# Kernel optimization log

Hardware: AMD Instinct MI355X
Metric: run time of the kernel (lower is better)

## Reference

```python
import jax, jax.numpy as jnp
import numpy as np

DEGREE = 5
LN_EPS = 1e-5


def _xavier(key, shape):
    fan_in, fan_out = shape[-1] if len(shape) == 2 else shape[1] * shape[2], shape[0]
    limit = float(np.sqrt(6.0 / (fan_in + fan_out)))
    return jax.random.uniform(key, shape, jnp.float32, -limit, limit)


def setup_inputs() -> dict:
    key = jax.random.key(0)
    ks = jax.random.split(key, 6)
    B, D0, D1, D2 = 16384, 1024, 1024, 512
    return {
        "x": jax.random.normal(ks[0], (B, D0), jnp.float32),
        "coeff1": _xavier(ks[1], (D1, D0, DEGREE + 1)),
        "base_w1": _xavier(ks[2], (D1, D0)),
        "bias1": jnp.zeros((D1,), jnp.float32),
        "ln_gamma": jnp.ones((D1,), jnp.float32),
        "ln_beta": jnp.zeros((D1,), jnp.float32),
        "coeff2": _xavier(ks[3], (D2, D1, DEGREE + 1)),
        "base_w2": _xavier(ks[4], (D2, D1)),
        "bias2": jnp.zeros((D2,), jnp.float32),
    }


def _cheb_layer(x, coeff, base_w, bias):
    # x: [B, I]; coeff: [O, I, D+1]; base_w: [O, I]; bias: [O]
    xn = jnp.tanh(x)
    polys = [jnp.ones_like(xn), xn]
    for _ in range(2, DEGREE + 1):
        polys.append(2.0 * xn * polys[-1] - polys[-2])
    cheb = jnp.stack(polys, axis=-1)  # [B, I, D+1]
    y = jnp.einsum("bid,oid->bo", cheb, coeff)
    y = y + x @ base_w.T + bias
    return y


def _layernorm(h, gamma, beta):
    mu = jnp.mean(h, axis=-1, keepdims=True)
    var = jnp.mean(jnp.square(h - mu), axis=-1, keepdims=True)
    return (h - mu) * jax.lax.rsqrt(var + LN_EPS) * gamma + beta


def reference(x, coeff1, base_w1, bias1, ln_gamma, ln_beta, coeff2, base_w2, bias2):
    x = jnp.tanh(x)  # input_normalization='tanh'
    h = _cheb_layer(x, coeff1, base_w1, bias1)
    h = _layernorm(h, ln_gamma, ln_beta)
    h = h * jax.nn.sigmoid(h)  # SiLU
    out = _cheb_layer(h, coeff2, base_w2, bias2)
    return out
```

## Files before the change

kernel.cpp:

```cpp
#include <hip/hip_runtime.h>


typedef __bf16 bf16x8 __attribute__((ext_vector_type(8)));
typedef float f32x4 __attribute__((ext_vector_type(4)));
typedef unsigned short u16x8 __attribute__((ext_vector_type(8)));

__device__ __forceinline__ unsigned short f2bf(float f) {
    unsigned int u = __float_as_uint(f);
    unsigned int r = (u + 0x7FFFu + ((u >> 16) & 1u)) >> 16;
    return (unsigned short)r;
}
__device__ __forceinline__ float bf2f(unsigned short b) {
    return __uint_as_float(((unsigned int)b) << 16);
}

__device__ __forceinline__ float fast_tanh(float x) {
    float a = fminf(fmaxf(x, -15.f), 15.f);
    float e = __expf(2.f * a);
    return 1.f - 2.f * __builtin_amdgcn_rcpf(e + 1.f);
}
__device__ __forceinline__ float fast_silu(float y) {
    float a = fminf(fmaxf(y, -30.f), 30.f);
    return y * __builtin_amdgcn_rcpf(1.f + __expf(-a));
}

__device__ __forceinline__ void cheb_pack(float s, unsigned short* o6) {
    float u  = fast_tanh(s);
    float T1 = u;
    float T2 = 2.f * u * u - 1.f;
    float T3 = 2.f * u * T2 - T1;
    float T4 = 2.f * u * T3 - T2;
    float T5 = 2.f * u * T4 - T3;
    o6[0] = f2bf(T1); o6[1] = f2bf(T2); o6[2] = f2bf(T3);
    o6[3] = f2bf(T4); o6[4] = f2bf(T5); o6[5] = f2bf(s);
}

__device__ __forceinline__ void load_lds16(const void* g, void* l) {
    __builtin_amdgcn_global_load_lds(
        (const __attribute__((address_space(1))) void*)g,
        (__attribute__((address_space(3))) void*)l, 16, 0, 0);
}

__global__ __launch_bounds__(256) void prep_w_kernel(
    const float* __restrict__ coeff, const float* __restrict__ base_w,
    unsigned short* __restrict__ W, int OI)
{
    int idx = blockIdx.x * 256 + threadIdx.x;
    if (idx >= OI) return;
    const float* c = coeff + (size_t)idx * 6;
    unsigned short w0 = f2bf(c[1]), w1 = f2bf(c[2]), w2 = f2bf(c[3]),
                   w3 = f2bf(c[4]), w4 = f2bf(c[5]), w5 = f2bf(base_w[idx]);
    unsigned int* d = (unsigned int*)(W + (size_t)idx * 6);
    d[0] = w0 | ((unsigned int)w1 << 16);
    d[1] = w2 | ((unsigned int)w3 << 16);
    d[2] = w4 | ((unsigned int)w5 << 16);
}

__global__ __launch_bounds__(256) void prep_bias_kernel(
    const float* __restrict__ coeff, const float* __restrict__ bias,
    float* __restrict__ bp, int I)
{
    int o = blockIdx.x, tid = threadIdx.x;
    float s = 0.f;
    for (int i = tid; i < I; i += 256) s += coeff[((size_t)o * I + i) * 6];
    #pragma unroll
    for (int off = 32; off > 0; off >>= 1) s += __shfl_down(s, off);
    __shared__ float red[4];
    int lane = tid & 63, wv = tid >> 6;
    if (lane == 0) red[wv] = s;
    __syncthreads();
    if (tid == 0) bp[o] = bias[o] + red[0] + red[1] + red[2] + red[3];
}

__global__ __launch_bounds__(256) void expand1_kernel(
    const float* __restrict__ x, unsigned short* __restrict__ Xa)
{
    int b = blockIdx.x, tid = threadIdx.x;
    f32x4 xv = *(const f32x4*)(x + (size_t)b * 1024 + tid * 4);
    alignas(16) unsigned short ov[24];
    #pragma unroll
    for (int e = 0; e < 4; e++) cheb_pack(fast_tanh(xv[e]), ov + e * 6);
    u16x8* dst = (u16x8*)(Xa + (size_t)b * 6144 + tid * 24);
    const u16x8* src = (const u16x8*)ov;
    dst[0] = src[0]; dst[1] = src[1]; dst[2] = src[2];
}

__global__ __launch_bounds__(256) void ln_silu_expand_kernel(
    const unsigned short* __restrict__ H, const float* __restrict__ gamma,
    const float* __restrict__ beta, unsigned short* __restrict__ Xa)
{
    int b = blockIdx.x, tid = threadIdx.x;
    ushort4 hb = *(const ushort4*)(H + (size_t)b * 1024 + tid * 4);
    float hv[4] = { bf2f(hb.x), bf2f(hb.y), bf2f(hb.z), bf2f(hb.w) };
    float s1 = hv[0] + hv[1] + hv[2] + hv[3];
    float s2 = hv[0]*hv[0] + hv[1]*hv[1] + hv[2]*hv[2] + hv[3]*hv[3];
    #pragma unroll
    for (int off = 32; off > 0; off >>= 1) {
        s1 += __shfl_down(s1, off);
        s2 += __shfl_down(s2, off);
    }
    __shared__ float red[8];
    __shared__ float stats[2];
    int lane = tid & 63, wv = tid >> 6;
    if (lane == 0) { red[wv] = s1; red[4 + wv] = s2; }
    __syncthreads();
    if (tid == 0) {
        float t1 = red[0] + red[1] + red[2] + red[3];
        float t2 = red[4] + red[5] + red[6] + red[7];
        float mu = t1 * (1.f / 1024.f);
        float var = t2 * (1.f / 1024.f) - mu * mu;
        stats[0] = mu;
        stats[1] = rsqrtf(var + 1e-5f);
    }
    __syncthreads();
    float mu = stats[0], rs = stats[1];
    f32x4 g  = *(const f32x4*)(gamma + tid * 4);
    f32x4 bt = *(const f32x4*)(beta  + tid * 4);
    alignas(16) unsigned short ov[24];
    #pragma unroll
    for (int e = 0; e < 4; e++) {
        float y = (hv[e] - mu) * rs * g[e] + bt[e];
        cheb_pack(fast_silu(y), ov + e * 6);
    }
    u16x8* dst = (u16x8*)(Xa + (size_t)b * 6144 + tid * 24);
    const u16x8* src = (const u16x8*)ov;
    dst[0] = src[0]; dst[1] = src[1]; dst[2] = src[2];
}

#define FENCE() asm volatile("" ::: "memory")

#define PH_MID() do { \
    FENCE(); __builtin_amdgcn_s_barrier(); \
    asm volatile("s_waitcnt lgkmcnt(0)" ::: "memory"); \
    __builtin_amdgcn_sched_barrier(0); \
    __builtin_amdgcn_s_setprio(1); } while (0)

#define PH_END() do { \
    __builtin_amdgcn_s_setprio(0); \
    FENCE(); __builtin_amdgcn_s_barrier(); FENCE(); } while (0)

#define VM_STEADY() do { \
    if constexpr (BN == 256) asm volatile("s_waitcnt vmcnt(8)" ::: "memory"); \
    else                     asm volatile("s_waitcnt vmcnt(6)" ::: "memory"); } while (0)
#define VM_DRAIN() asm volatile("s_waitcnt vmcnt(0)" ::: "memory")

#define RD_A(DST0, DST1, BASE, MH) do { \
    _Pragma("unroll") \
    for (int mf = 0; mf < 4; ++mf) { \
        const unsigned short* p_ = (BASE) + ((MH) * 64 + mf * 16) * 64; \
        DST0[mf] = *(const bf16x8*)(p_ + c0); \
        DST1[mf] = *(const bf16x8*)(p_ + c1); \
    } } while (0)

#define RD_B(DST, BASE, CSEL) do { \
    _Pragma("unroll") \
    for (int nf = 0; nf < FN; ++nf) \
        DST[nf] = *(const bf16x8*)((BASE) + (nf * 16) * 64 + (CSEL)); \
    } while (0)

#define QUAD(MH, AV, BV) do { \
    _Pragma("unroll") \
    for (int mf = 0; mf < 4; ++mf) \
        _Pragma("unroll") \
        for (int nf = 0; nf < FN; ++nf) \
            acc[MH][mf][nf] = __builtin_amdgcn_mfma_f32_16x16x32_bf16( \
                AV[mf], BV[nf], acc[MH][mf][nf], 0, 0, 0); \
    } while (0)

template<int BN, bool OUT_BF16>
__global__ __launch_bounds__(512, 2) void gemm8_kernel(
    const unsigned short* __restrict__ A,
    const unsigned short* __restrict__ Wt,
    const float* __restrict__ bias,
    void* __restrict__ Cout,
    int N, int K, int NMT)
{
    constexpr int FN   = BN / 64;
    constexpr int BUPW = BN / 64;

    __shared__ __align__(16) unsigned short As[2 * 256 * 64];
    __shared__ __align__(16) unsigned short Bs[2 * BN * 64];

    const int tid  = threadIdx.x;
    const int lane = tid & 63;
    const int wave = tid >> 6;
    const int wm   = wave >> 2;
    const int wn   = wave & 3;

    int wg = blockIdx.x;
    {
        const int nwg = gridDim.x;
        if ((nwg & 7) == 0) {
            const int cpx = nwg >> 3;
            wg = (wg & 7) * cpx + (wg >> 3);
        }
    }
    const int mt = wg % NMT;
    const int nt = wg / NMT;
    const size_t m0 = (size_t)mt * 256;
    const size_t n0 = (size_t)nt * BN;

    const int srow   = lane >> 3;
    const int schunk = (lane & 7) ^ (srow & 7);
    const unsigned short* Ag = A  + (m0 + srow) * (size_t)K + schunk * 8;
    const unsigned short* Bg = Wt + (n0 + srow) * (size_t)K + schunk * 8;

    const int fr  = lane & 15;
    const int cg  = lane >> 4;
    const int fr7 = fr & 7;
    const int c0  = ((cg    ) ^ fr7) << 3;
    const int c1  = ((cg + 4) ^ fr7) << 3;

    const int NT = K >> 6;

    const unsigned short* A0f = As + fr * 64 + (wm * 128) * 64;
    const unsigned short* A1f = A0f + 256 * 64;
    const unsigned short* B0f = Bs + fr * 64 + (wn * (BN / 4)) * 64;
    const unsigned short* B1f = B0f + BN * 64;

    auto stageA = [&](int kt, int bsel) {
        const unsigned short* g = Ag + kt * 64;
        unsigned short* l = As + bsel * (256 * 64);
        #pragma unroll
        for (int j = 0; j < 4; ++j) {
            const int u = wave * 4 + j;
            load_lds16(g + (size_t)(u * 8) * K, l + u * 512);
        }
    };
    auto stageB = [&](int kt, int bsel) {
        const unsigned short* g = Bg + kt * 64;
        unsigned short* l = Bs + bsel * (BN * 64);
        #pragma unroll
        for (int j = 0; j < BUPW; ++j) {
            const int u = wave * BUPW + j;
            load_lds16(g + (size_t)(u * 8) * K, l + u * 512);
        }
    };

    f32x4 acc[2][4][FN];
    #pragma unroll
    for (int mh = 0; mh < 2; ++mh)
        #pragma unroll
        for (int mf = 0; mf < 4; ++mf)
            #pragma unroll
            for (int nf = 0; nf < FN; ++nf)
                acc[mh][mf][nf] = f32x4{0.f, 0.f, 0.f, 0.f};

    stageB(0, 0); stageA(0, 0);
    stageB(1, 1); stageA(1, 1);
    VM_STEADY();
    FENCE(); __builtin_amdgcn_s_barrier(); FENCE();

    for (int kt = 0; kt < NT; kt += 2) {
        const bool st = (kt + 4) <= NT;
        bf16x8 a0[4], a1[4], b0[FN], b1[FN];

        RD_A(a0, a1, A0f, 0);
        RD_B(b0, B0f, c0);
        PH_MID(); QUAD(0, a0, b0); PH_END();

        RD_B(b1, B0f, c1);
        PH_MID(); QUAD(0, a1, b1); PH_END();

        RD_A(a0, a1, A0f, 1);
        if (st) stageB(kt + 2, 0);
        PH_MID(); QUAD(1, a0, b0); PH_END();

        if (st) { stageA(kt + 2, 0); VM_STEADY(); }
        else    { VM_DRAIN(); }
        PH_MID(); QUAD(1, a1, b1); PH_END();

        RD_A(a0, a1, A1f, 0);
        RD_B(b0, B1f, c0);
        PH_MID(); QUAD(0, a0, b0); PH_END();

        RD_B(b1, B1f, c1);
        PH_MID(); QUAD(0, a1, b1); PH_END();

        RD_A(a0, a1, A1f, 1);
        if (st) stageB(kt + 3, 1);
        PH_MID(); QUAD(1, a0, b0); PH_END();

        if (st) { stageA(kt + 3, 1); VM_STEADY(); }
        else    { VM_DRAIN(); }
        PH_MID(); QUAD(1, a1, b1); PH_END();
    }

    const size_t rbase0 = m0 + wm * 128 + ((lane >> 4) << 2);
    const int cb = lane & 15;
    int colg[FN]; float bv[FN];
    #pragma unroll
    for (int nf = 0; nf < FN; ++nf) {
        colg[nf] = (int)n0 + wn * (BN / 4) + nf * 16 + cb;
        bv[nf] = bias[colg[nf]];
    }
    #pragma unroll
    for (int mh = 0; mh < 2; ++mh)
        #pragma unroll
        for (int mf = 0; mf < 4; ++mf) {
            const size_t rg0 = rbase0 + mh * 64 + mf * 16;
            #pragma unroll
            for (int r = 0; r < 4; ++r) {
                const size_t rowoff = (rg0 + r) * (size_t)N;
                #pragma unroll
                for (int nf = 0; nf < FN; ++nf) {
                    const float v = acc[mh][mf][nf][r] + bv[nf];
                    if constexpr (OUT_BF16)
                        ((unsigned short*)Cout)[rowoff + colg[nf]] = f2bf(v);
                    else
                        ((float*)Cout)[rowoff + colg[nf]] = v;
                }
            }
        }
}

extern "C" void kernel_launch(void* const* d_in, const int* in_sizes, int n_in,
                              void* d_out, int out_size, void* d_ws, size_t ws_size,
                              hipStream_t stream)
{
    const float* x       = (const float*)d_in[0];
    const float* coeff1  = (const float*)d_in[1];
    const float* base_w1 = (const float*)d_in[2];
    const float* bias1   = (const float*)d_in[3];
    const float* gamma   = (const float*)d_in[4];
    const float* beta    = (const float*)d_in[5];
    const float* coeff2  = (const float*)d_in[6];
    const float* base_w2 = (const float*)d_in[7];
    const float* bias2   = (const float*)d_in[8];
    float* out = (float*)d_out;

    const int B = 16384, D0 = 1024, D1 = 1024, D2 = 512;
    const int K1 = D0 * 6, K2 = D1 * 6;

    char* base = (char*)d_ws;
    size_t off = 0;
    unsigned short* W1 = (unsigned short*)(base + off); off += (size_t)D1 * K1 * 2;
    unsigned short* W2 = (unsigned short*)(base + off); off += (size_t)D2 * K2 * 2;
    float* b1p = (float*)(base + off); off += (size_t)D1 * 4;
    float* b2p = (float*)(base + off); off += (size_t)D2 * 4;
    off = (off + 255) & ~(size_t)255;

    size_t per_row = (size_t)K1 * 2 + (size_t)D1 * 2;
    long long avail = (long long)ws_size - (long long)off;
    long long mcl = avail > 0 ? avail / (long long)per_row : 0;
    int Mc = (int)((mcl / 256) * 256);
    if (Mc < 256) Mc = 256;
    if (Mc > B) Mc = B;

    unsigned short* Xa = (unsigned short*)(base + off);
    unsigned short* h = (unsigned short*)(base + off + (size_t)Mc * K1 * 2);

    prep_w_kernel<<<(D1 * D0 + 255) / 256, 256, 0, stream>>>(coeff1, base_w1, W1, D1 * D0);
    prep_w_kernel<<<(D2 * D1 + 255) / 256, 256, 0, stream>>>(coeff2, base_w2, W2, D2 * D1);
    prep_bias_kernel<<<D1, 256, 0, stream>>>(coeff1, bias1, b1p, D0);
    prep_bias_kernel<<<D2, 256, 0, stream>>>(coeff2, bias2, b2p, D1);

    for (int m0 = 0; m0 < B; m0 += Mc) {
        int rows = (B - m0 < Mc) ? (B - m0) : Mc;
        int nmt = rows / 256;
        expand1_kernel<<<rows, 256, 0, stream>>>(x + (size_t)m0 * D0, Xa);
        gemm8_kernel<256, true><<<nmt * (D1 / 256), 512, 0, stream>>>(
            Xa, W1, b1p, h, D1, K1, nmt);
        ln_silu_expand_kernel<<<rows, 256, 0, stream>>>(h, gamma, beta, Xa);
        gemm8_kernel<128, false><<<nmt * (D2 / 128), 512, 0, stream>>>(
            Xa, W2, b2p, out + (size_t)m0 * D2, D2, K2, nmt);
    }
}
```

Measured before the change: 678.8 us.

## Replace 8-phase GEMM schedule with simpler BK=32 double-buffered pipeline

Swaps the GEMM mainloop's 8-phase ping-pong schedule (BK=64, barriers and setprio around each MFMA quad) for a simpler loop with BK=32 tiles, two LDS buffers and register double-buffering of fragments. Each iteration waits for all outstanding loads, prefetches the next tile into registers and issues async global->LDS loads for a tile two steps ahead. The LDS layout and swizzle change to 32-wide rows. This halves the LDS footprint and cuts barrier overhead, but it issues full vmcnt(0) waits every step and exposes less latency per barrier.

```diff
diff --git a/kernel.cpp b/kernel.cpp
--- a/kernel.cpp
+++ b/kernel.cpp
@@ -127,59 +127,24 @@
     dst[0] = src[0]; dst[1] = src[1]; dst[2] = src[2];
 }
 
-#define FENCE() asm volatile("" ::: "memory")
-
-#define PH_MID() do { \
-    FENCE(); __builtin_amdgcn_s_barrier(); \
-    asm volatile("s_waitcnt lgkmcnt(0)" ::: "memory"); \
-    __builtin_amdgcn_sched_barrier(0); \
-    __builtin_amdgcn_s_setprio(1); } while (0)
-
-#define PH_END() do { \
-    __builtin_amdgcn_s_setprio(0); \
-    FENCE(); __builtin_amdgcn_s_barrier(); FENCE(); } while (0)
-
-#define VM_STEADY() do { \
-    if constexpr (BN == 256) asm volatile("s_waitcnt vmcnt(8)" ::: "memory"); \
-    else                     asm volatile("s_waitcnt vmcnt(6)" ::: "memory"); } while (0)
-#define VM_DRAIN() asm volatile("s_waitcnt vmcnt(0)" ::: "memory")
-
-#define RD_A(DST0, DST1, BASE, MH) do { \
-    _Pragma("unroll") \
-    for (int mf = 0; mf < 4; ++mf) { \
-        const unsigned short* p_ = (BASE) + ((MH) * 64 + mf * 16) * 64; \
-        DST0[mf] = *(const bf16x8*)(p_ + c0); \
-        DST1[mf] = *(const bf16x8*)(p_ + c1); \
-    } } while (0)
-
-#define RD_B(DST, BASE, CSEL) do { \
-    _Pragma("unroll") \
-    for (int nf = 0; nf < FN; ++nf) \
-        DST[nf] = *(const bf16x8*)((BASE) + (nf * 16) * 64 + (CSEL)); \
-    } while (0)
-
-#define QUAD(MH, AV, BV) do { \
-    _Pragma("unroll") \
-    for (int mf = 0; mf < 4; ++mf) \
-        _Pragma("unroll") \
-        for (int nf = 0; nf < FN; ++nf) \
-            acc[MH][mf][nf] = __builtin_amdgcn_mfma_f32_16x16x32_bf16( \
-                AV[mf], BV[nf], acc[MH][mf][nf], 0, 0, 0); \
-    } while (0)
+
+#define WAITTOP() do { \
+    asm volatile("s_waitcnt vmcnt(0) lgkmcnt(0)" ::: "memory"); \
+    __builtin_amdgcn_s_barrier(); } while (0)
 
 template<int BN, bool OUT_BF16>
-__global__ __launch_bounds__(512, 2) void gemm8_kernel(
+__global__ __launch_bounds__(512, 2) void gemm3_kernel(
     const unsigned short* __restrict__ A,
     const unsigned short* __restrict__ Wt,
     const float* __restrict__ bias,
     void* __restrict__ Cout,
     int N, int K, int NMT)
 {
-    constexpr int FN   = BN / 64;
-    constexpr int BUPW = BN / 64;
-
-    __shared__ __align__(16) unsigned short As[2 * 256 * 64];
-    __shared__ __align__(16) unsigned short Bs[2 * BN * 64];
+    constexpr int FN  = BN / 64;
+    constexpr int ASZ = 256 * 32;
+    constexpr int BSZ = BN * 32;
+    __shared__ __align__(16) unsigned short As[2 * ASZ];
+    __shared__ __align__(16) unsigned short Bs[2 * BSZ];
 
     const int tid  = threadIdx.x;
     const int lane = tid & 63;
@@ -190,52 +155,32 @@
     int wg = blockIdx.x;
     {
         const int nwg = gridDim.x;
-        if ((nwg & 7) == 0) {
-            const int cpx = nwg >> 3;
-            wg = (wg & 7) * cpx + (wg >> 3);
-        }
+        if ((nwg & 7) == 0) { const int cpx = nwg >> 3; wg = (wg & 7) * cpx + (wg >> 3); }
     }
     const int mt = wg % NMT;
     const int nt = wg / NMT;
     const size_t m0 = (size_t)mt * 256;
     const size_t n0 = (size_t)nt * BN;
 
-    const int srow   = lane >> 3;
-    const int schunk = (lane & 7) ^ (srow & 7);
-    const unsigned short* Ag = A  + (m0 + srow) * (size_t)K + schunk * 8;
-    const unsigned short* Bg = Wt + (n0 + srow) * (size_t)K + schunk * 8;
-
-    const int fr  = lane & 15;
-    const int cg  = lane >> 4;
-    const int fr7 = fr & 7;
-    const int c0  = ((cg    ) ^ fr7) << 3;
-    const int c1  = ((cg + 4) ^ fr7) << 3;
-
-    const int NT = K >> 6;
-
-    const unsigned short* A0f = As + fr * 64 + (wm * 128) * 64;
-    const unsigned short* A1f = A0f + 256 * 64;
-    const unsigned short* B0f = Bs + fr * 64 + (wn * (BN / 4)) * 64;
-    const unsigned short* B1f = B0f + BN * 64;
-
-    auto stageA = [&](int kt, int bsel) {
-        const unsigned short* g = Ag + kt * 64;
-        unsigned short* l = As + bsel * (256 * 64);
-        #pragma unroll
-        for (int j = 0; j < 4; ++j) {
-            const int u = wave * 4 + j;
-            load_lds16(g + (size_t)(u * 8) * K, l + u * 512);
-        }
-    };
-    auto stageB = [&](int kt, int bsel) {
-        const unsigned short* g = Bg + kt * 64;
-        unsigned short* l = Bs + bsel * (BN * 64);
-        #pragma unroll
-        for (int j = 0; j < BUPW; ++j) {
-            const int u = wave * BUPW + j;
-            load_lds16(g + (size_t)(u * 8) * K, l + u * 512);
-        }
-    };
+    const int cs   = (((lane & 3) ^ ((lane >> 3) & 3)) << 3);
+    const int srow = lane >> 2;
+    const unsigned short* AgJ0 = A + (m0 + (size_t)((wave * 2 + 0) * 16 + srow)) * K + cs;
+    const unsigned short* AgJ1 = A + (m0 + (size_t)((wave * 2 + 1) * 16 + srow)) * K + cs;
+    const unsigned short* BgJ0 = Wt + (n0 + (size_t)((wave * (BN / 128) + 0) * 16 + srow)) * K + cs;
+    const unsigned short* BgJ1 = (BN == 256)
+        ? Wt + (n0 + (size_t)((wave * 2 + 1) * 16 + srow)) * K + cs : BgJ0;
+    unsigned short* AD0 = As + (wave * 2 + 0) * 512 + lane * 8;
+    unsigned short* AD1 = As + (wave * 2 + 1) * 512 + lane * 8;
+    unsigned short* BD0 = Bs + (wave * (BN / 128) + 0) * 512 + lane * 8;
+    unsigned short* BD1 = Bs + (wave * 2 + 1) * 512 + lane * 8;
+
+    const int fr = lane & 15;
+    const int cg = lane >> 4;
+    const int ck = ((cg ^ ((fr >> 1) & 3)) << 3);
+    const unsigned short* PA = As + (wm * 128 + fr) * 32 + ck;
+    const unsigned short* PB = Bs + (wn * (BN / 4) + fr) * 32 + ck;
+
+    const int NT = K >> 5;
 
     f32x4 acc[2][4][FN];
     #pragma unroll
@@ -246,45 +191,64 @@
             for (int nf = 0; nf < FN; ++nf)
                 acc[mh][mf][nf] = f32x4{0.f, 0.f, 0.f, 0.f};
 
-    stageB(0, 0); stageA(0, 0);
-    stageB(1, 1); stageA(1, 1);
-    VM_STEADY();
-    FENCE(); __builtin_amdgcn_s_barrier(); FENCE();
-
-    for (int kt = 0; kt < NT; kt += 2) {
-        const bool st = (kt + 4) <= NT;
-        bf16x8 a0[4], a1[4], b0[FN], b1[FN];
-
-        RD_A(a0, a1, A0f, 0);
-        RD_B(b0, B0f, c0);
-        PH_MID(); QUAD(0, a0, b0); PH_END();
-
-        RD_B(b1, B0f, c1);
-        PH_MID(); QUAD(0, a1, b1); PH_END();
-
-        RD_A(a0, a1, A0f, 1);
-        if (st) stageB(kt + 2, 0);
-        PH_MID(); QUAD(1, a0, b0); PH_END();
-
-        if (st) { stageA(kt + 2, 0); VM_STEADY(); }
-        else    { VM_DRAIN(); }
-        PH_MID(); QUAD(1, a1, b1); PH_END();
-
-        RD_A(a0, a1, A1f, 0);
-        RD_B(b0, B1f, c0);
-        PH_MID(); QUAD(0, a0, b0); PH_END();
-
-        RD_B(b1, B1f, c1);
-        PH_MID(); QUAD(0, a1, b1); PH_END();
-
-        RD_A(a0, a1, A1f, 1);
-        if (st) stageB(kt + 3, 1);
-        PH_MID(); QUAD(1, a0, b0); PH_END();
-
-        if (st) { stageA(kt + 3, 1); VM_STEADY(); }
-        else    { VM_DRAIN(); }
-        PH_MID(); QUAD(1, a1, b1); PH_END();
-    }
+    bf16x8 aF[8], aG[8], bF[FN], bG[FN];
+
+#define STAGE(T, B_) do { \
+    const size_t ko_ = (size_t)(T) * 32; \
+    load_lds16(AgJ0 + ko_, AD0 + (B_) * ASZ); \
+    load_lds16(AgJ1 + ko_, AD1 + (B_) * ASZ); \
+    load_lds16(BgJ0 + ko_, BD0 + (B_) * BSZ); \
+    if constexpr (BN == 256) load_lds16(BgJ1 + ko_, BD1 + (B_) * BSZ); \
+} while (0)
+
+#define RD(AF_, BF_, B_) do { \
+    _Pragma("unroll") \
+    for (int mh = 0; mh < 2; ++mh) \
+        _Pragma("unroll") \
+        for (int mf = 0; mf < 4; ++mf) \
+            AF_[mh * 4 + mf] = *(const bf16x8*)(PA + (B_) * ASZ + (mh * 64 + mf * 16) * 32); \
+    _Pragma("unroll") \
+    for (int nf = 0; nf < FN; ++nf) \
+        BF_[nf] = *(const bf16x8*)(PB + (B_) * BSZ + nf * 16 * 32); \
+} while (0)
+
+#define MM(AF_, BF_) do { \
+    _Pragma("unroll") \
+    for (int mh = 0; mh < 2; ++mh) \
+        _Pragma("unroll") \
+        for (int mf = 0; mf < 4; ++mf) \
+            _Pragma("unroll") \
+            for (int nf = 0; nf < FN; ++nf) \
+                acc[mh][mf][nf] = __builtin_amdgcn_mfma_f32_16x16x32_bf16( \
+                    AF_[mh * 4 + mf], BF_[nf], acc[mh][mf][nf], 0, 0, 0); \
+} while (0)
+
+    STAGE(0, 0);
+    STAGE(1, 1);
+    if constexpr (BN == 256) asm volatile("s_waitcnt vmcnt(4)" ::: "memory");
+    else                     asm volatile("s_waitcnt vmcnt(3)" ::: "memory");
+    __builtin_amdgcn_s_barrier();
+    RD(aF, bF, 0);
+
+    for (int t = 0; t < NT - 2; t += 2) {
+        WAITTOP();
+        RD(aG, bG, 1);
+        STAGE(t + 2, 0);
+        MM(aF, bF);
+        WAITTOP();
+        RD(aF, bF, 0);
+        STAGE(t + 3, 1);
+        MM(aG, bG);
+    }
+    WAITTOP();
+    RD(aG, bG, 1);
+    MM(aF, bF);
+    WAITTOP();
+    MM(aG, bG);
+
+#undef STAGE
+#undef RD
+#undef MM
 
     const size_t rbase0 = m0 + wm * 128 + ((lane >> 4) << 2);
     const int cb = lane & 15;
@@ -359,10 +323,10 @@
         int rows = (B - m0 < Mc) ? (B - m0) : Mc;
         int nmt = rows / 256;
         expand1_kernel<<<rows, 256, 0, stream>>>(x + (size_t)m0 * D0, Xa);
-        gemm8_kernel<256, true><<<nmt * (D1 / 256), 512, 0, stream>>>(
+        gemm3_kernel<256, true><<<nmt * (D1 / 256), 512, 0, stream>>>(
             Xa, W1, b1p, h, D1, K1, nmt);
         ln_silu_expand_kernel<<<rows, 256, 0, stream>>>(h, gamma, beta, Xa);
-        gemm8_kernel<128, false><<<nmt * (D2 / 128), 512, 0, stream>>>(
+        gemm3_kernel<128, false><<<nmt * (D2 / 128), 512, 0, stream>>>(
             Xa, W2, b2p, out + (size_t)m0 * D2, D2, K2, nmt);
     }
 }
```

Result: slower. 714.8 us (+5.3%).
